# Kernel tuning notes

Hardware: AMD Instinct MI355X
Metric: run time of the kernel (lower is better)

## Reference

```python
import jax, jax.numpy as jnp
import numpy as np

H = 16  # hidden size


def _gru_dir(x_tbi, Wih, Whh, bih, bhh, reverse):
    """Single-direction GRU over time. x_tbi: [T,B,I]. Returns [T,B,H] outputs
    aligned to original time positions (lax.scan reverse matches torch's
    bidirectional alignment). PyTorch gate order: r, z, n."""
    B = x_tbi.shape[1]
    h0 = jnp.zeros((B, Whh.shape[1]), x_tbi.dtype)
    # Precompute all input projections in one big GEMM: [T,B,3H]
    gi_all = jnp.einsum('tbi,gi->tbg', x_tbi, Wih) + bih

    def step(h, gi):
        gh = h @ Whh.T + bhh                     # [B,3H]
        i_r, i_z, i_n = jnp.split(gi, 3, axis=-1)
        h_r, h_z, h_n = jnp.split(gh, 3, axis=-1)
        r = jax.nn.sigmoid(i_r + h_r)
        z = jax.nn.sigmoid(i_z + h_z)
        n = jnp.tanh(i_n + r * h_n)
        h_new = (1.0 - z) * n + z * h
        return h_new, h_new

    _, ys = jax.lax.scan(step, h0, gi_all, reverse=reverse)
    return ys  # [T,B,H]


def _bigru_layer(x_tbi, pf, pb):
    yf = _gru_dir(x_tbi, pf[0], pf[1], pf[2], pf[3], False)
    yb = _gru_dir(x_tbi, pb[0], pb[1], pb[2], pb[3], True)
    return jnp.concatenate([yf, yb], axis=-1)  # [T,B,2H]


def setup_inputs() -> dict:
    key = jax.random.key(0)
    ks = jax.random.split(key, 20)
    B, T, I = 4096, 512, 1
    bound = 1.0 / np.sqrt(H)  # torch default init U(-1/sqrt(H), 1/sqrt(H))

    def u(k, shape):
        return jax.random.uniform(k, shape, jnp.float32, -bound, bound)

    inp = {'x': jax.random.normal(ks[0], (B, T, I), jnp.float32)}
    # layer 0: input dim 1; layer 1: input dim 2H=32. Suffix f=forward, b=backward.
    dims = {0: I, 1: 2 * H}
    i = 1
    for l in (0, 1):
        for d in ('f', 'b'):
            inp[f'W_ih_l{l}_{d}'] = u(ks[i], (3 * H, dims[l])); i += 1
            inp[f'W_hh_l{l}_{d}'] = u(ks[i], (3 * H, H)); i += 1
            inp[f'b_ih_l{l}_{d}'] = u(ks[i], (3 * H,)); i += 1
            inp[f'b_hh_l{l}_{d}'] = u(ks[i], (3 * H,)); i += 1
    return inp


def reference(x,
              W_ih_l0_f, W_hh_l0_f, b_ih_l0_f, b_hh_l0_f,
              W_ih_l0_b, W_hh_l0_b, b_ih_l0_b, b_hh_l0_b,
              W_ih_l1_f, W_hh_l1_f, b_ih_l1_f, b_hh_l1_f,
              W_ih_l1_b, W_hh_l1_b, b_ih_l1_b, b_hh_l1_b):
    x_tbi = jnp.transpose(x.astype(jnp.float32), (1, 0, 2))  # [T,B,1]
    y0 = _bigru_layer(x_tbi,
                      (W_ih_l0_f, W_hh_l0_f, b_ih_l0_f, b_hh_l0_f),
                      (W_ih_l0_b, W_hh_l0_b, b_ih_l0_b, b_hh_l0_b))
    y1 = _bigru_layer(y0,
                      (W_ih_l1_f, W_hh_l1_f, b_ih_l1_f, b_hh_l1_f),
                      (W_ih_l1_b, W_hh_l1_b, b_ih_l1_b, b_hh_l1_b))
    # out[:, -1, :] in batch_first layout == last time step of [T,B,2H]
    return y1[-1]  # [B, 2H]
```

## Files before the change

### kernel.cpp

```cpp
#include <hip/hip_runtime.h>
#include <hip/hip_fp16.h>

typedef _Float16 v2h __attribute__((ext_vector_type(2)));
typedef _Float16 h4t __attribute__((ext_vector_type(4)));
typedef _Float16 h8t __attribute__((ext_vector_type(8)));
typedef float f4t __attribute__((ext_vector_type(4)));

static constexpr int T = 512;
static constexpr int B = 4096;

__device__ __forceinline__ float frcp_(float x) { return __builtin_amdgcn_rcpf(x); }
__device__ __forceinline__ float sig_(float x) { return frcp_(1.0f + __expf(-x)); }
__device__ __forceinline__ float tanh_(float x) { return 1.0f - 2.0f * frcp_(1.0f + __expf(2.0f * x)); }

#define WAVE_SYNC() do { asm volatile("" ::: "memory"); \
                         __builtin_amdgcn_wave_barrier(); \
                         asm volatile("" ::: "memory"); } while (0)

__device__ __forceinline__ v2h as_h2_(unsigned u) {
    union { unsigned u; v2h h; } c; c.u = u; return c.h;
}

__device__ __forceinline__ h4t pack4_(float a, float b, float c, float d) {
    auto p0 = __builtin_amdgcn_cvt_pkrtz(a, b);
    auto p1 = __builtin_amdgcn_cvt_pkrtz(c, d);
    union { struct { decltype(p0) a, b; } p; h4t h; } cv;
    cv.p.a = p0; cv.p.b = p1;
    return cv.h;
}

__global__ void __launch_bounds__(256, 2) k_l0(
    const float* __restrict__ x,
    const float* __restrict__ Wf, const float* __restrict__ Uf,
    const float* __restrict__ bif, const float* __restrict__ bhf,
    const float* __restrict__ Wb, const float* __restrict__ Ub,
    const float* __restrict__ bib, const float* __restrict__ bhb,
    __half* __restrict__ y0f,
    __half* __restrict__ y0b)
{
    __shared__ __half hbuf[256];
    const int tid  = threadIdx.x;
    const int j    = tid & 15;
    const int dir  = (tid >> 4) & 1;
    const int s    = tid >> 5;
    const int unit = tid >> 4;
    const int b    = blockIdx.x * 8 + s;
    __half* hb = hbuf + unit * 16;

    const float* Wih = dir ? Wb : Wf;
    const float* Whh = dir ? Ub : Uf;
    const float* bih = dir ? bib : bif;
    const float* bhh = dir ? bhb : bhf;

    v2h wr[8], wz[8], wn[8];
#pragma unroll
    for (int q = 0; q < 8; ++q) {
        wr[q] = (v2h){ (_Float16)Whh[j * 16 + 2 * q],
                       (_Float16)Whh[j * 16 + 2 * q + 1] };
        wz[q] = (v2h){ (_Float16)Whh[(16 + j) * 16 + 2 * q],
                       (_Float16)Whh[(16 + j) * 16 + 2 * q + 1] };
        wn[q] = (v2h){ (_Float16)Whh[(32 + j) * 16 + 2 * q],
                       (_Float16)Whh[(32 + j) * 16 + 2 * q + 1] };
    }
    const float wxr  = Wih[j], wxz = Wih[16 + j], wxn = Wih[32 + j];
    const float br   = bih[j] + bhh[j];
    const float bz   = bih[16 + j] + bhh[16 + j];
    const float bin_ = bih[32 + j];
    const float bhn  = bhh[32 + j];

    const int t0   = dir ? (T - 1) : 0;
    const int step = dir ? -1 : 1;
    const float* xp = x + (size_t)b * T + t0;
    __half* yp = (dir ? y0b : y0f) + ((size_t)t0 * B + b) * 16 + j;
    const ptrdiff_t ystep = (ptrdiff_t)step * B * 16;

    hb[j] = __half(0.0f);
    WAVE_SYNC();

    float xv = xp[0];
    float x1 = xp[step];
    const float* xq = xp + 2 * step;
    float hj = 0.0f;

    for (int it = 0; it < T; ++it) {
        float x2 = *xq;
        if (it < T - 3) xq += step;
        const uint4* hp = reinterpret_cast<const uint4*>(hb);
        uint4 u0 = hp[0], u1 = hp[1];
        const unsigned hw[8] = { u0.x, u0.y, u0.z, u0.w, u1.x, u1.y, u1.z, u1.w };
        float ar = fmaf(xv, wxr, br);
        float az = fmaf(xv, wxz, bz);
        float hn = bhn;
#pragma unroll
        for (int q = 0; q < 8; ++q) {
            v2h hh = as_h2_(hw[q]);
            ar = __builtin_amdgcn_fdot2(hh, wr[q], ar, false);
            az = __builtin_amdgcn_fdot2(hh, wz[q], az, false);
            hn = __builtin_amdgcn_fdot2(hh, wn[q], hn, false);
        }
        float r = sig_(ar), z = sig_(az);
        float n = tanh_(fmaf(r, hn, fmaf(xv, wxn, bin_)));
        hj = fmaf(z, hj - n, n);
        __half hf = __float2half(hj);
        *yp = hf;
        yp += ystep;
        WAVE_SYNC();
        hb[j] = hf;
        WAVE_SYNC();
        xv = x1; x1 = x2;
    }
}

__global__ void __launch_bounds__(64, 1) k_l1m(
    const __half* __restrict__ y0f, const __half* __restrict__ y0b,
    const float* __restrict__ Wih1, const float* __restrict__ Whh1,
    const float* __restrict__ bih1, const float* __restrict__ bhh1,
    const float* __restrict__ Wih1b,
    const float* __restrict__ bih1b, const float* __restrict__ bhh1b,
    float* __restrict__ out)
{
    const int lane = threadIdx.x & 63;
    const int c = lane & 15;
    const int g = lane >> 4;
    const int b = blockIdx.x * 16 + c;

    h8t Air, Aiz, Ain;
    {
        const float* pr = Wih1 + (size_t)c * 32 + 8 * g;
        const float* pz = Wih1 + (size_t)(16 + c) * 32 + 8 * g;
        const float* pn = Wih1 + (size_t)(32 + c) * 32 + 8 * g;
#pragma unroll
        for (int e = 0; e < 8; ++e) {
            Air[e] = (_Float16)pr[e];
            Aiz[e] = (_Float16)pz[e];
            Ain[e] = (_Float16)pn[e];
        }
    }
    h4t Ahr, Ahz, Ahn;
    {
        const float* pr = Whh1 + (size_t)c * 16 + 4 * g;
        const float* pz = Whh1 + (size_t)(16 + c) * 16 + 4 * g;
        const float* pn = Whh1 + (size_t)(32 + c) * 16 + 4 * g;
#pragma unroll
        for (int e = 0; e < 4; ++e) {
            Ahr[e] = (_Float16)pr[e];
            Ahz[e] = (_Float16)pz[e];
            Ahn[e] = (_Float16)pn[e];
        }
    }
    f4t Crb, Czb, Cnb, Chn, Z4;
#pragma unroll
    for (int i = 0; i < 4; ++i) {
        const int row = 4 * g + i;
        Crb[i] = bih1[row] + bhh1[row];
        Czb[i] = bih1[16 + row] + bhh1[16 + row];
        Cnb[i] = bih1[32 + row];
        Chn[i] = bhh1[32 + row];
        Z4[i]  = 0.0f;
    }

    const __half* ysrc = (g < 2) ? y0f : y0b;
    const uint4* yp = reinterpret_cast<const uint4*>(
        ysrc + (size_t)b * 16 + (size_t)(g & 1) * 8);
    const size_t ystr = (size_t)B * 2;

    uint4 buf[8];
#pragma unroll
    for (int i = 0; i < 8; ++i) buf[i] = yp[(size_t)i * ystr];

    float h[4] = {0.0f, 0.0f, 0.0f, 0.0f};
    h4t Bh = {};

#pragma unroll 8
    for (int it = 0; it < T; ++it) {
        uint4 ya = buf[it & 7];
        const size_t tn = (it + 8 < T) ? (size_t)(it + 8) : (size_t)(T - 1);
        buf[it & 7] = yp[tn * ystr];
        h8t By;
        { union { uint4 u; h8t h; } cv; cv.u = ya; By = cv.h; }
        f4t Dr = __builtin_amdgcn_mfma_f32_16x16x32_f16(Air, By, Crb, 0, 0, 0);
        f4t Dz = __builtin_amdgcn_mfma_f32_16x16x32_f16(Aiz, By, Czb, 0, 0, 0);
        f4t Dn = __builtin_amdgcn_mfma_f32_16x16x32_f16(Ain, By, Cnb, 0, 0, 0);
        f4t Er = __builtin_amdgcn_mfma_f32_16x16x16f16(Ahr, Bh, Z4, 0, 0, 0);
        f4t Ez = __builtin_amdgcn_mfma_f32_16x16x16f16(Ahz, Bh, Z4, 0, 0, 0);
        f4t En = __builtin_amdgcn_mfma_f32_16x16x16f16(Ahn, Bh, Chn, 0, 0, 0);
#pragma unroll
        for (int i = 0; i < 4; ++i) {
            float r = sig_(Dr[i] + Er[i]);
            float z = sig_(Dz[i] + Ez[i]);
            float n = tanh_(fmaf(r, En[i], Dn[i]));
            h[i] = fmaf(z, h[i] - n, n);
        }
        Bh = pack4_(h[0], h[1], h[2], h[3]);
    }

#pragma unroll
    for (int i = 0; i < 4; ++i)
        out[(size_t)b * 32 + 4 * g + i] = h[i];

    uint4 yfin = buf[(T - 1) & 7];
    h8t Abr, Abz, Abn;
    {
        const float* pr = Wih1b + (size_t)c * 32 + 8 * g;
        const float* pz = Wih1b + (size_t)(16 + c) * 32 + 8 * g;
        const float* pn = Wih1b + (size_t)(32 + c) * 32 + 8 * g;
#pragma unroll
        for (int e = 0; e < 8; ++e) {
            Abr[e] = (_Float16)pr[e];
            Abz[e] = (_Float16)pz[e];
            Abn[e] = (_Float16)pn[e];
        }
    }
    f4t Cbr, Cbz, Cbn;
    float ghn[4];
#pragma unroll
    for (int i = 0; i < 4; ++i) {
        const int row = 4 * g + i;
        Cbr[i] = bih1b[row] + bhh1b[row];
        Cbz[i] = bih1b[16 + row] + bhh1b[16 + row];
        Cbn[i] = bih1b[32 + row];
        ghn[i] = bhh1b[32 + row];
    }
    h8t By;
    { union { uint4 u; h8t h; } cv; cv.u = yfin; By = cv.h; }
    f4t Dr = __builtin_amdgcn_mfma_f32_16x16x32_f16(Abr, By, Cbr, 0, 0, 0);
    f4t Dz = __builtin_amdgcn_mfma_f32_16x16x32_f16(Abz, By, Cbz, 0, 0, 0);
    f4t Dn = __builtin_amdgcn_mfma_f32_16x16x32_f16(Abn, By, Cbn, 0, 0, 0);
#pragma unroll
    for (int i = 0; i < 4; ++i) {
        float r = sig_(Dr[i]);
        float z = sig_(Dz[i]);
        float n = tanh_(fmaf(r, ghn[i], Dn[i]));
        out[(size_t)b * 32 + 16 + 4 * g + i] = (1.0f - z) * n;
    }
}

extern "C" void kernel_launch(void* const* d_in, const int* in_sizes, int n_in,
                              void* d_out, int out_size, void* d_ws, size_t ws_size,
                              hipStream_t stream) {
    const float* x     = (const float*)d_in[0];
    const float* Wih0f = (const float*)d_in[1];
    const float* Whh0f = (const float*)d_in[2];
    const float* bih0f = (const float*)d_in[3];
    const float* bhh0f = (const float*)d_in[4];
    const float* Wih0b = (const float*)d_in[5];
    const float* Whh0b = (const float*)d_in[6];
    const float* bih0b = (const float*)d_in[7];
    const float* bhh0b = (const float*)d_in[8];
    const float* Wih1f = (const float*)d_in[9];
    const float* Whh1f = (const float*)d_in[10];
    const float* bih1f = (const float*)d_in[11];
    const float* bhh1f = (const float*)d_in[12];
    const float* Wih1b = (const float*)d_in[13];
    const float* bih1b = (const float*)d_in[15];
    const float* bhh1b = (const float*)d_in[16];

    __half* y0f = (__half*)d_ws;
    __half* y0b = y0f + (size_t)T * B * 16;
    float* out = (float*)d_out;

    hipLaunchKernelGGL(k_l0, dim3(B * 2 / 16), dim3(256), 0, stream,
                       x, Wih0f, Whh0f, bih0f, bhh0f,
                       Wih0b, Whh0b, bih0b, bhh0b, y0f, y0b);
    hipLaunchKernelGGL(k_l1m, dim3(B / 16), dim3(64), 0, stream,
                       y0f, y0b, Wih1f, Whh1f, bih1f, bhh1f,
                       Wih1b, bih1b, bhh1b, out);
}
```

Baseline: 278.9 us.

## Fuse layer-0 forward GRU into layer-1 MFMA kernel and fold gate scaling into weights

The layer-0 forward direction is now computed inside the layer-1 kernel with MFMA, one step ahead of layer 1, so its outputs are never written to or read back from global memory. Layer 0 backward still runs as a separate kernel that writes y0b. The sigmoid and tanh scale factors are folded into the weights and biases, so the activations use exp2 directly and skip a multiply. In exchange, the fused kernel's serial per-step chain is longer, with nine dependent MFMAs plus two activation blocks per step.

```diff
diff --git a/kernel.cpp b/kernel.cpp
--- a/kernel.cpp
+++ b/kernel.cpp
@@ -3,15 +3,24 @@
 
 typedef _Float16 v2h __attribute__((ext_vector_type(2)));
 typedef _Float16 h4t __attribute__((ext_vector_type(4)));
-typedef _Float16 h8t __attribute__((ext_vector_type(8)));
 typedef float f4t __attribute__((ext_vector_type(4)));
 
 static constexpr int T = 512;
 static constexpr int B = 4096;
 
+static constexpr float SG = -1.4426950408889634f;
+static constexpr float SN = -2.8853900817779268f;
+
 __device__ __forceinline__ float frcp_(float x) { return __builtin_amdgcn_rcpf(x); }
-__device__ __forceinline__ float sig_(float x) { return frcp_(1.0f + __expf(-x)); }
-__device__ __forceinline__ float tanh_(float x) { return 1.0f - 2.0f * frcp_(1.0f + __expf(2.0f * x)); }
+__device__ __forceinline__ float exp2_(float x) {
+#if __has_builtin(__builtin_amdgcn_exp2f)
+    return __builtin_amdgcn_exp2f(x);
+#else
+    return __expf(x * 0.69314718055994531f);
+#endif
+}
+__device__ __forceinline__ float sigp_(float p) { return frcp_(1.0f + exp2_(p)); }
+__device__ __forceinline__ float tanhp_(float p) { return fmaf(2.0f, frcp_(1.0f + exp2_(p)), -1.0f); }
 
 #define WAVE_SYNC() do { asm volatile("" ::: "memory"); \
                          __builtin_amdgcn_wave_barrier(); \
@@ -19,6 +28,9 @@
 
 __device__ __forceinline__ v2h as_h2_(unsigned u) {
     union { unsigned u; v2h h; } c; c.u = u; return c.h;
+}
+__device__ __forceinline__ h4t as_h4_(uint2 u) {
+    union { uint2 u; h4t h; } c; c.u = u; return c.h;
 }
 
 __device__ __forceinline__ h4t pack4_(float a, float b, float c, float d) {
@@ -29,68 +41,55 @@
     return cv.h;
 }
 
-__global__ void __launch_bounds__(256, 2) k_l0(
+__global__ void __launch_bounds__(256, 2) k_l0b(
     const float* __restrict__ x,
-    const float* __restrict__ Wf, const float* __restrict__ Uf,
-    const float* __restrict__ bif, const float* __restrict__ bhf,
     const float* __restrict__ Wb, const float* __restrict__ Ub,
     const float* __restrict__ bib, const float* __restrict__ bhb,
-    __half* __restrict__ y0f,
     __half* __restrict__ y0b)
 {
     __shared__ __half hbuf[256];
     const int tid  = threadIdx.x;
     const int j    = tid & 15;
-    const int dir  = (tid >> 4) & 1;
-    const int s    = tid >> 5;
     const int unit = tid >> 4;
-    const int b    = blockIdx.x * 8 + s;
+    const int b    = blockIdx.x * 16 + unit;
     __half* hb = hbuf + unit * 16;
 
-    const float* Wih = dir ? Wb : Wf;
-    const float* Whh = dir ? Ub : Uf;
-    const float* bih = dir ? bib : bif;
-    const float* bhh = dir ? bhb : bhf;
-
     v2h wr[8], wz[8], wn[8];
 #pragma unroll
     for (int q = 0; q < 8; ++q) {
-        wr[q] = (v2h){ (_Float16)Whh[j * 16 + 2 * q],
-                       (_Float16)Whh[j * 16 + 2 * q + 1] };
-        wz[q] = (v2h){ (_Float16)Whh[(16 + j) * 16 + 2 * q],
-                       (_Float16)Whh[(16 + j) * 16 + 2 * q + 1] };
-        wn[q] = (v2h){ (_Float16)Whh[(32 + j) * 16 + 2 * q],
-                       (_Float16)Whh[(32 + j) * 16 + 2 * q + 1] };
-    }
-    const float wxr  = Wih[j], wxz = Wih[16 + j], wxn = Wih[32 + j];
-    const float br   = bih[j] + bhh[j];
-    const float bz   = bih[16 + j] + bhh[16 + j];
-    const float bin_ = bih[32 + j];
-    const float bhn  = bhh[32 + j];
-
-    const int t0   = dir ? (T - 1) : 0;
-    const int step = dir ? -1 : 1;
-    const float* xp = x + (size_t)b * T + t0;
-    __half* yp = (dir ? y0b : y0f) + ((size_t)t0 * B + b) * 16 + j;
-    const ptrdiff_t ystep = (ptrdiff_t)step * B * 16;
+        wr[q] = (v2h){ (_Float16)(SG * Ub[j * 16 + 2 * q]),
+                       (_Float16)(SG * Ub[j * 16 + 2 * q + 1]) };
+        wz[q] = (v2h){ (_Float16)(SG * Ub[(16 + j) * 16 + 2 * q]),
+                       (_Float16)(SG * Ub[(16 + j) * 16 + 2 * q + 1]) };
+        wn[q] = (v2h){ (_Float16)(SN * Ub[(32 + j) * 16 + 2 * q]),
+                       (_Float16)(SN * Ub[(32 + j) * 16 + 2 * q + 1]) };
+    }
+    const float wxr  = SG * Wb[j], wxz = SG * Wb[16 + j], wxn = SN * Wb[32 + j];
+    const float br   = SG * (bib[j] + bhb[j]);
+    const float bz   = SG * (bib[16 + j] + bhb[16 + j]);
+    const float bin_ = SN * bib[32 + j];
+    const float bhn  = SN * bhb[32 + j];
+
+    const float* xp = x + (size_t)b * T + (T - 1);
+    __half* yp = y0b + ((size_t)(T - 1) * B + b) * 16 + j;
 
     hb[j] = __half(0.0f);
     WAVE_SYNC();
 
     float xv = xp[0];
-    float x1 = xp[step];
-    const float* xq = xp + 2 * step;
+    float x1 = xp[-1];
+    const float* xq = xp - 2;
     float hj = 0.0f;
 
     for (int it = 0; it < T; ++it) {
         float x2 = *xq;
-        if (it < T - 3) xq += step;
+        if (it < T - 3) xq -= 1;
         const uint4* hp = reinterpret_cast<const uint4*>(hb);
         uint4 u0 = hp[0], u1 = hp[1];
-        const unsigned hw[8] = { u0.x, u0.y, u0.z, u0.w, u1.x, u1.y, u1.z, u1.w };
         float ar = fmaf(xv, wxr, br);
         float az = fmaf(xv, wxz, bz);
         float hn = bhn;
+        const unsigned hw[8] = { u0.x, u0.y, u0.z, u0.w, u1.x, u1.y, u1.z, u1.w };
 #pragma unroll
         for (int q = 0; q < 8; ++q) {
             v2h hh = as_h2_(hw[q]);
@@ -98,12 +97,12 @@
             az = __builtin_amdgcn_fdot2(hh, wz[q], az, false);
             hn = __builtin_amdgcn_fdot2(hh, wn[q], hn, false);
         }
-        float r = sig_(ar), z = sig_(az);
-        float n = tanh_(fmaf(r, hn, fmaf(xv, wxn, bin_)));
+        float r = sigp_(ar), z = sigp_(az);
+        float n = tanhp_(fmaf(r, hn, fmaf(xv, wxn, bin_)));
         hj = fmaf(z, hj - n, n);
         __half hf = __float2half(hj);
         *yp = hf;
-        yp += ystep;
+        yp -= (ptrdiff_t)B * 16;
         WAVE_SYNC();
         hb[j] = hf;
         WAVE_SYNC();
@@ -111,12 +110,15 @@
     }
 }
 
-__global__ void __launch_bounds__(64, 1) k_l1m(
-    const __half* __restrict__ y0f, const __half* __restrict__ y0b,
+__global__ void __launch_bounds__(64, 1) k_fused(
+    const float* __restrict__ x,
+    const float* __restrict__ Wih0, const float* __restrict__ Whh0,
+    const float* __restrict__ bih0, const float* __restrict__ bhh0,
     const float* __restrict__ Wih1, const float* __restrict__ Whh1,
     const float* __restrict__ bih1, const float* __restrict__ bhh1,
     const float* __restrict__ Wih1b,
     const float* __restrict__ bih1b, const float* __restrict__ bhh1b,
+    const __half* __restrict__ y0b,
     float* __restrict__ out)
 {
     const int lane = threadIdx.x & 63;
@@ -124,113 +126,175 @@
     const int g = lane >> 4;
     const int b = blockIdx.x * 16 + c;
 
-    h8t Air, Aiz, Ain;
-    {
-        const float* pr = Wih1 + (size_t)c * 32 + 8 * g;
-        const float* pz = Wih1 + (size_t)(16 + c) * 32 + 8 * g;
-        const float* pn = Wih1 + (size_t)(32 + c) * 32 + 8 * g;
-#pragma unroll
-        for (int e = 0; e < 8; ++e) {
-            Air[e] = (_Float16)pr[e];
-            Aiz[e] = (_Float16)pz[e];
-            Ain[e] = (_Float16)pn[e];
-        }
-    }
-    h4t Ahr, Ahz, Ahn;
-    {
-        const float* pr = Whh1 + (size_t)c * 16 + 4 * g;
-        const float* pz = Whh1 + (size_t)(16 + c) * 16 + 4 * g;
-        const float* pn = Whh1 + (size_t)(32 + c) * 16 + 4 * g;
-#pragma unroll
-        for (int e = 0; e < 4; ++e) {
-            Ahr[e] = (_Float16)pr[e];
-            Ahz[e] = (_Float16)pz[e];
-            Ahn[e] = (_Float16)pn[e];
-        }
-    }
-    f4t Crb, Czb, Cnb, Chn, Z4;
+    h4t A0r, A0z, A0n;
+#pragma unroll
+    for (int e = 0; e < 4; ++e) {
+        A0r[e] = (_Float16)(SG * Whh0[(size_t)c * 16 + 4 * g + e]);
+        A0z[e] = (_Float16)(SG * Whh0[(size_t)(16 + c) * 16 + 4 * g + e]);
+        A0n[e] = (_Float16)(SN * Whh0[(size_t)(32 + c) * 16 + 4 * g + e]);
+    }
+    float sgwxr[4], sgwxz[4], snwxn[4], br0[4], bz0[4], bn0[4];
+    f4t Chn0;
 #pragma unroll
     for (int i = 0; i < 4; ++i) {
         const int row = 4 * g + i;
-        Crb[i] = bih1[row] + bhh1[row];
-        Czb[i] = bih1[16 + row] + bhh1[16 + row];
-        Cnb[i] = bih1[32 + row];
-        Chn[i] = bhh1[32 + row];
-        Z4[i]  = 0.0f;
-    }
-
-    const __half* ysrc = (g < 2) ? y0f : y0b;
-    const uint4* yp = reinterpret_cast<const uint4*>(
-        ysrc + (size_t)b * 16 + (size_t)(g & 1) * 8);
-    const size_t ystr = (size_t)B * 2;
-
-    uint4 buf[8];
-#pragma unroll
-    for (int i = 0; i < 8; ++i) buf[i] = yp[(size_t)i * ystr];
-
-    float h[4] = {0.0f, 0.0f, 0.0f, 0.0f};
-    h4t Bh = {};
-
-#pragma unroll 8
-    for (int it = 0; it < T; ++it) {
-        uint4 ya = buf[it & 7];
-        const size_t tn = (it + 8 < T) ? (size_t)(it + 8) : (size_t)(T - 1);
-        buf[it & 7] = yp[tn * ystr];
-        h8t By;
-        { union { uint4 u; h8t h; } cv; cv.u = ya; By = cv.h; }
-        f4t Dr = __builtin_amdgcn_mfma_f32_16x16x32_f16(Air, By, Crb, 0, 0, 0);
-        f4t Dz = __builtin_amdgcn_mfma_f32_16x16x32_f16(Aiz, By, Czb, 0, 0, 0);
-        f4t Dn = __builtin_amdgcn_mfma_f32_16x16x32_f16(Ain, By, Cnb, 0, 0, 0);
-        f4t Er = __builtin_amdgcn_mfma_f32_16x16x16f16(Ahr, Bh, Z4, 0, 0, 0);
-        f4t Ez = __builtin_amdgcn_mfma_f32_16x16x16f16(Ahz, Bh, Z4, 0, 0, 0);
-        f4t En = __builtin_amdgcn_mfma_f32_16x16x16f16(Ahn, Bh, Chn, 0, 0, 0);
+        sgwxr[i] = SG * Wih0[row];
+        sgwxz[i] = SG * Wih0[16 + row];
+        snwxn[i] = SN * Wih0[32 + row];
+        br0[i] = SG * (bih0[row] + bhh0[row]);
+        bz0[i] = SG * (bih0[16 + row] + bhh0[16 + row]);
+        bn0[i] = SN * bih0[32 + row];
+        Chn0[i] = SN * bhh0[32 + row];
+    }
+
+    h4t P0r, P0z, P0n, Pyr, Pyz, Pyn, U1r, U1z, U1n;
+#pragma unroll
+    for (int e = 0; e < 4; ++e) {
+        const int k = 4 * g + e;
+        P0r[e] = (_Float16)(SG * Wih1[(size_t)c * 32 + k]);
+        P0z[e] = (_Float16)(SG * Wih1[(size_t)(16 + c) * 32 + k]);
+        P0n[e] = (_Float16)(SN * Wih1[(size_t)(32 + c) * 32 + k]);
+        Pyr[e] = (_Float16)(SG * Wih1[(size_t)c * 32 + 16 + k]);
+        Pyz[e] = (_Float16)(SG * Wih1[(size_t)(16 + c) * 32 + 16 + k]);
+        Pyn[e] = (_Float16)(SN * Wih1[(size_t)(32 + c) * 32 + 16 + k]);
+        U1r[e] = (_Float16)(SG * Whh1[(size_t)c * 16 + k]);
+        U1z[e] = (_Float16)(SG * Whh1[(size_t)(16 + c) * 16 + k]);
+        U1n[e] = (_Float16)(SN * Whh1[(size_t)(32 + c) * 16 + k]);
+    }
+    f4t Crb, Czb, Cnb, Chn1;
+#pragma unroll
+    for (int i = 0; i < 4; ++i) {
+        const int row = 4 * g + i;
+        Crb[i] = SG * (bih1[row] + bhh1[row]);
+        Czb[i] = SG * (bih1[16 + row] + bhh1[16 + row]);
+        Cnb[i] = SN * bih1[32 + row];
+        Chn1[i] = SN * bhh1[32 + row];
+    }
+
+    const uint2* yq = reinterpret_cast<const uint2*>(y0b) + (size_t)b * 4 + g;
+    const size_t ystr = (size_t)B * 4;
+    uint2 buf[4];
+    buf[0] = yq[0];
+    buf[1] = yq[0];
+    buf[2] = yq[ystr];
+    buf[3] = yq[2 * ystr];
+
+    const float* xp = x + (size_t)b * T;
+    float x_cur = xp[0];
+    float x_nxt = xp[1];
+    const float* xq2 = xp + 2;
+
+    float h0[4] = {0.0f, 0.0f, 0.0f, 0.0f};
+    float h1[4] = {0.0f, 0.0f, 0.0f, 0.0f};
+    h4t Bh0 = {}, Bh1 = {};
+
+    for (int ito = 0; ito < T / 4; ++ito) {
+#pragma unroll
+        for (int u = 0; u < 4; ++u) {
+            const int it = ito * 4 + u;
+            uint2 yau = buf[u];
+            const size_t tn = (it + 3 < T) ? (size_t)(it + 3) : (size_t)(T - 1);
+            buf[u] = yq[tn * ystr];
+            float x2 = *xq2;
+            if (it < T - 3) xq2 += 1;
+
+            f4t C0r, C0z;
+            float inx[4];
+#pragma unroll
+            for (int i = 0; i < 4; ++i) {
+                C0r[i] = fmaf(x_cur, sgwxr[i], br0[i]);
+                C0z[i] = fmaf(x_cur, sgwxz[i], bz0[i]);
+                inx[i] = fmaf(x_cur, snwxn[i], bn0[i]);
+            }
+            f4t E0r = __builtin_amdgcn_mfma_f32_16x16x16f16(A0r, Bh0, C0r, 0, 0, 0);
+            f4t E0z = __builtin_amdgcn_mfma_f32_16x16x16f16(A0z, Bh0, C0z, 0, 0, 0);
+            f4t E0n = __builtin_amdgcn_mfma_f32_16x16x16f16(A0n, Bh0, Chn0, 0, 0, 0);
+
+            h4t By = as_h4_(yau);
+            f4t D1r = __builtin_amdgcn_mfma_f32_16x16x16f16(P0r, Bh0, Crb, 0, 0, 0);
+            f4t D1z = __builtin_amdgcn_mfma_f32_16x16x16f16(P0z, Bh0, Czb, 0, 0, 0);
+            f4t D1n = __builtin_amdgcn_mfma_f32_16x16x16f16(P0n, Bh0, Cnb, 0, 0, 0);
+            D1r = __builtin_amdgcn_mfma_f32_16x16x16f16(Pyr, By, D1r, 0, 0, 0);
+            D1z = __builtin_amdgcn_mfma_f32_16x16x16f16(Pyz, By, D1z, 0, 0, 0);
+            D1n = __builtin_amdgcn_mfma_f32_16x16x16f16(Pyn, By, D1n, 0, 0, 0);
+            f4t E1r = __builtin_amdgcn_mfma_f32_16x16x16f16(U1r, Bh1, D1r, 0, 0, 0);
+            f4t E1z = __builtin_amdgcn_mfma_f32_16x16x16f16(U1z, Bh1, D1z, 0, 0, 0);
+            f4t E1n = __builtin_amdgcn_mfma_f32_16x16x16f16(U1n, Bh1, Chn1, 0, 0, 0);
+
+#pragma unroll
+            for (int i = 0; i < 4; ++i) {
+                float r = sigp_(E0r[i]);
+                float z = sigp_(E0z[i]);
+                float n = tanhp_(fmaf(r, E0n[i], inx[i]));
+                h0[i] = fmaf(z, h0[i] - n, n);
+            }
+#pragma unroll
+            for (int i = 0; i < 4; ++i) {
+                float r = sigp_(E1r[i]);
+                float z = sigp_(E1z[i]);
+                float n = tanhp_(fmaf(r, E1n[i], D1n[i]));
+                float hv = fmaf(z, h1[i] - n, n);
+                h1[i] = (it == 0) ? 0.0f : hv;
+            }
+            Bh0 = pack4_(h0[0], h0[1], h0[2], h0[3]);
+            Bh1 = pack4_(h1[0], h1[1], h1[2], h1[3]);
+            x_cur = x_nxt; x_nxt = x2;
+        }
+    }
+
+    h4t Byf = as_h4_(buf[(T - 1) & 3]);
+    {
+        f4t D1r = __builtin_amdgcn_mfma_f32_16x16x16f16(P0r, Bh0, Crb, 0, 0, 0);
+        f4t D1z = __builtin_amdgcn_mfma_f32_16x16x16f16(P0z, Bh0, Czb, 0, 0, 0);
+        f4t D1n = __builtin_amdgcn_mfma_f32_16x16x16f16(P0n, Bh0, Cnb, 0, 0, 0);
+        D1r = __builtin_amdgcn_mfma_f32_16x16x16f16(Pyr, Byf, D1r, 0, 0, 0);
+        D1z = __builtin_amdgcn_mfma_f32_16x16x16f16(Pyz, Byf, D1z, 0, 0, 0);
+        D1n = __builtin_amdgcn_mfma_f32_16x16x16f16(Pyn, Byf, D1n, 0, 0, 0);
+        f4t E1r = __builtin_amdgcn_mfma_f32_16x16x16f16(U1r, Bh1, D1r, 0, 0, 0);
+        f4t E1z = __builtin_amdgcn_mfma_f32_16x16x16f16(U1z, Bh1, D1z, 0, 0, 0);
+        f4t E1n = __builtin_amdgcn_mfma_f32_16x16x16f16(U1n, Bh1, Chn1, 0, 0, 0);
 #pragma unroll
         for (int i = 0; i < 4; ++i) {
-            float r = sig_(Dr[i] + Er[i]);
-            float z = sig_(Dz[i] + Ez[i]);
-            float n = tanh_(fmaf(r, En[i], Dn[i]));
-            h[i] = fmaf(z, h[i] - n, n);
+            float r = sigp_(E1r[i]);
+            float z = sigp_(E1z[i]);
+            float n = tanhp_(fmaf(r, E1n[i], D1n[i]));
+            h1[i] = fmaf(z, h1[i] - n, n);
+            out[(size_t)b * 32 + 4 * g + i] = h1[i];
         }
-        Bh = pack4_(h[0], h[1], h[2], h[3]);
-    }
-
-#pragma unroll
-    for (int i = 0; i < 4; ++i)
-        out[(size_t)b * 32 + 4 * g + i] = h[i];
-
-    uint4 yfin = buf[(T - 1) & 7];
-    h8t Abr, Abz, Abn;
-    {
-        const float* pr = Wih1b + (size_t)c * 32 + 8 * g;
-        const float* pz = Wih1b + (size_t)(16 + c) * 32 + 8 * g;
-        const float* pn = Wih1b + (size_t)(32 + c) * 32 + 8 * g;
-#pragma unroll
-        for (int e = 0; e < 8; ++e) {
-            Abr[e] = (_Float16)pr[e];
-            Abz[e] = (_Float16)pz[e];
-            Abn[e] = (_Float16)pn[e];
-        }
+    }
+
+    h4t Qb0r, Qb0z, Qb0n, Qbyr, Qbyz, Qbyn;
+#pragma unroll
+    for (int e = 0; e < 4; ++e) {
+        const int k = 4 * g + e;
+        Qb0r[e] = (_Float16)(SG * Wih1b[(size_t)c * 32 + k]);
+        Qb0z[e] = (_Float16)(SG * Wih1b[(size_t)(16 + c) * 32 + k]);
+        Qb0n[e] = (_Float16)(SN * Wih1b[(size_t)(32 + c) * 32 + k]);
+        Qbyr[e] = (_Float16)(SG * Wih1b[(size_t)c * 32 + 16 + k]);
+        Qbyz[e] = (_Float16)(SG * Wih1b[(size_t)(16 + c) * 32 + 16 + k]);
+        Qbyn[e] = (_Float16)(SN * Wih1b[(size_t)(32 + c) * 32 + 16 + k]);
     }
     f4t Cbr, Cbz, Cbn;
     float ghn[4];
 #pragma unroll
     for (int i = 0; i < 4; ++i) {
         const int row = 4 * g + i;
-        Cbr[i] = bih1b[row] + bhh1b[row];
-        Cbz[i] = bih1b[16 + row] + bhh1b[16 + row];
-        Cbn[i] = bih1b[32 + row];
-        ghn[i] = bhh1b[32 + row];
-    }
-    h8t By;
-    { union { uint4 u; h8t h; } cv; cv.u = yfin; By = cv.h; }
-    f4t Dr = __builtin_amdgcn_mfma_f32_16x16x32_f16(Abr, By, Cbr, 0, 0, 0);
-    f4t Dz = __builtin_amdgcn_mfma_f32_16x16x32_f16(Abz, By, Cbz, 0, 0, 0);
-    f4t Dn = __builtin_amdgcn_mfma_f32_16x16x32_f16(Abn, By, Cbn, 0, 0, 0);
+        Cbr[i] = SG * (bih1b[row] + bhh1b[row]);
+        Cbz[i] = SG * (bih1b[16 + row] + bhh1b[16 + row]);
+        Cbn[i] = SN * bih1b[32 + row];
+        ghn[i] = SN * bhh1b[32 + row];
+    }
+    f4t Gr = __builtin_amdgcn_mfma_f32_16x16x16f16(Qb0r, Bh0, Cbr, 0, 0, 0);
+    f4t Gz = __builtin_amdgcn_mfma_f32_16x16x16f16(Qb0z, Bh0, Cbz, 0, 0, 0);
+    f4t Gn = __builtin_amdgcn_mfma_f32_16x16x16f16(Qb0n, Bh0, Cbn, 0, 0, 0);
+    Gr = __builtin_amdgcn_mfma_f32_16x16x16f16(Qbyr, Byf, Gr, 0, 0, 0);
+    Gz = __builtin_amdgcn_mfma_f32_16x16x16f16(Qbyz, Byf, Gz, 0, 0, 0);
+    Gn = __builtin_amdgcn_mfma_f32_16x16x16f16(Qbyn, Byf, Gn, 0, 0, 0);
 #pragma unroll
     for (int i = 0; i < 4; ++i) {
-        float r = sig_(Dr[i]);
-        float z = sig_(Dz[i]);
-        float n = tanh_(fmaf(r, ghn[i], Dn[i]));
+        float r = sigp_(Gr[i]);
+        float z = sigp_(Gz[i]);
+        float n = tanhp_(fmaf(r, ghn[i], Gn[i]));
         out[(size_t)b * 32 + 16 + 4 * g + i] = (1.0f - z) * n;
     }
 }
@@ -255,14 +319,13 @@
     const float* bih1b = (const float*)d_in[15];
     const float* bhh1b = (const float*)d_in[16];
 
-    __half* y0f = (__half*)d_ws;
-    __half* y0b = y0f + (size_t)T * B * 16;
+    __half* y0b = (__half*)d_ws;
     float* out = (float*)d_out;
 
-    hipLaunchKernelGGL(k_l0, dim3(B * 2 / 16), dim3(256), 0, stream,
+    hipLaunchKernelGGL(k_l0b, dim3(B / 16), dim3(256), 0, stream,
+                       x, Wih0b, Whh0b, bih0b, bhh0b, y0b);
+    hipLaunchKernelGGL(k_fused, dim3(B / 16), dim3(64), 0, stream,
                        x, Wih0f, Whh0f, bih0f, bhh0f,
-                       Wih0b, Whh0b, bih0b, bhh0b, y0f, y0b);
-    hipLaunchKernelGGL(k_l1m, dim3(B / 16), dim3(64), 0, stream,
-                       y0f, y0b, Wih1f, Whh1f, bih1f, bhh1f,
-                       Wih1b, bih1b, bhh1b, out);
-}
+                       Wih1f, Whh1f, bih1f, bhh1f,
+                       Wih1b, bih1b, bhh1b, y0b, out);
+}
```

Result: slower. 323.2 us (+15.9%).
